# Performance work log

Measured on AMD Instinct MI355X. Metric: run time of the kernel, lower is better.

Reference implementation:

```python
import jax, jax.numpy as jnp
import numpy as np

N = 100000
E = 1600000
IN_C = 128
HID = 64
HEADS = 2
OUT_C = 64
Z = 16
NEG_SLOPE = 0.2


def _gat_layer(x, src, dst, W, a_src, a_dst, b, heads, d):
    # x: [N, in], W: [in, heads*d]
    h = (x @ W).reshape(-1, heads, d)                      # [N, H, d]
    alpha_s = (h * a_src).sum(-1)                          # [N, H]
    alpha_d = (h * a_dst).sum(-1)                          # [N, H]
    e = jax.nn.leaky_relu(alpha_s[src] + alpha_d[dst], NEG_SLOPE)  # [E, H]
    m = jax.ops.segment_max(e, dst, num_segments=N)        # [N, H]
    ex = jnp.exp(e - m[dst])
    denom = jax.ops.segment_sum(ex, dst, num_segments=N)   # [N, H]
    alpha = ex / (denom[dst] + 1e-16)                      # [E, H]
    out = jax.ops.segment_sum(h[src] * alpha[:, :, None], dst, num_segments=N)  # [N, H, d]
    return out.reshape(-1, heads * d) + b


def setup_inputs() -> dict:
    key = jax.random.key(0)
    ks = jax.random.split(key, 24)
    g = lambda k, shp, fan: jax.random.normal(k, shp, jnp.float32) * (1.0 / np.sqrt(fan))
    inp = {
        "x": jax.random.normal(ks[0], (N, IN_C), jnp.float32),
        "edge_index": jax.random.randint(ks[1], (2, E), 0, N, jnp.int64),
        "edge_attr": jax.random.normal(ks[2], (E, 8), jnp.float32),
        "eps": jax.random.normal(ks[3], (N, Z), jnp.float32),
        # GAT layer 1: heads=2, d=HID
        "W1": g(ks[4], (IN_C, HEADS * HID), IN_C),
        "a_src1": g(ks[5], (HEADS, HID), HID),
        "a_dst1": g(ks[6], (HEADS, HID), HID),
        "b1": jnp.zeros((HEADS * HID,), jnp.float32),
        # GAT layer 2: heads=1, d=OUT_C
        "W2": g(ks[7], (HEADS * HID, OUT_C), HEADS * HID),
        "a_src2": g(ks[8], (1, OUT_C), OUT_C),
        "a_dst2": g(ks[9], (1, OUT_C), OUT_C),
        "b2": jnp.zeros((OUT_C,), jnp.float32),
        # VAE
        "fc1_w": g(ks[10], (64, 128), 64), "fc1_b": jnp.zeros((128,), jnp.float32),
        "mu_w": g(ks[11], (128, Z), 128), "mu_b": jnp.zeros((Z,), jnp.float32),
        "lv_w": g(ks[12], (128, Z), 128), "lv_b": jnp.zeros((Z,), jnp.float32),
        "fc3_w": g(ks[13], (Z, 128), Z), "fc3_b": jnp.zeros((128,), jnp.float32),
        "fc4_w": g(ks[14], (128, 64), 128), "fc4_b": jnp.zeros((64,), jnp.float32),
    }
    return inp


def reference(x, edge_index, edge_attr, eps, W1, a_src1, a_dst1, b1, W2, a_src2, a_dst2, b2,
              fc1_w, fc1_b, mu_w, mu_b, lv_w, lv_b, fc3_w, fc3_b, fc4_w, fc4_b):
    src, dst = edge_index[0], edge_index[1]
    # GAT stack (edge_attr ignored: GATConv edge_dim=None)
    h = jax.nn.relu(_gat_layer(x, src, dst, W1, a_src1, a_dst1, b1, HEADS, HID))
    gat_out = _gat_layer(h, src, dst, W2, a_src2, a_dst2, b2, 1, OUT_C)  # [N, 64]
    # VAE
    h1 = jax.nn.relu(gat_out @ fc1_w + fc1_b)
    mu = h1 @ mu_w + mu_b
    logvar = h1 @ lv_w + lv_b
    lv = jnp.clip(logvar, -10.0, 10.0)
    z = mu + eps * jnp.exp(0.5 * lv)
    h3 = jax.nn.relu(z @ fc3_w + fc3_b)
    recon = h3 @ fc4_w + fc4_b
    return recon, mu, logvar, gat_out
```

## Files before the change

kernel.cpp:

```cpp
#include <hip/hip_runtime.h>
#include <hip/hip_bf16.h>

typedef __attribute__((ext_vector_type(8))) short bf16x8;
typedef __attribute__((ext_vector_type(4))) float f32x4;

__device__ __forceinline__ unsigned short f2b_bits(float x) {
    __hip_bfloat16 h = __float2bfloat16(x);
    unsigned short u;
    __builtin_memcpy(&u, &h, 2);
    return u;
}
__device__ __forceinline__ unsigned int pack2(float a, float b) {
    return (unsigned int)f2b_bits(a) | ((unsigned int)f2b_bits(b) << 16);
}
__device__ __forceinline__ float sx8(unsigned int w, int b) {
    return (float)((int)(w << (24 - 8 * b)) >> 24);
}

template<int FIN, int FOUT, int EPI, int HD, bool ABF, int ACT>
__global__ __launch_bounds__(256) void mfma_k(const void* __restrict__ Av,
                                              const float* __restrict__ W,
                                              const float* __restrict__ W2,
                                              const float* __restrict__ bias,
                                              const float* __restrict__ bias2,
                                              void* __restrict__ outv,
                                              void* __restrict__ out2,
                                              void* __restrict__ out3,
                                              float* __restrict__ scales,
                                              const float* __restrict__ asr,
                                              const float* __restrict__ adr,
                                              float* __restrict__ aso,
                                              float* __restrict__ ado,
                                              const float* __restrict__ epsp,
                                              int n)
{
    constexpr int KE = (FIN < 32) ? 32 : FIN;
    constexpr int KP = KE + 8;
    constexpr int KS = KE / 32;
    constexpr int NT = FOUT / 16;
    __shared__ __align__(16) unsigned short As[64 * KP];
    __shared__ __align__(16) unsigned short Wt[FOUT * KP];

    const int t  = threadIdx.x;
    const int m0 = blockIdx.x * 64;

    for (int idx = t; idx < 64 * (KE / 4); idx += 256) {
        int r  = idx / (KE / 4);
        int c4 = (idx % (KE / 4)) * 4;
        int row = m0 + r;
        unsigned int p0 = 0, p1 = 0;
        if (row < n && c4 < FIN) {
            if constexpr (ABF) {
                uint2 rv = *(const uint2*)((const unsigned short*)Av + (size_t)row * FIN + c4);
                p0 = rv.x; p1 = rv.y;
            } else {
                float4 v = *(const float4*)((const float*)Av + (size_t)row * FIN + c4);
                p0 = pack2(v.x, v.y); p1 = pack2(v.z, v.w);
            }
        }
        *(uint2*)(As + r * KP + c4) = make_uint2(p0, p1);
    }
    for (int idx = t; idx < KE * (FOUT / 4); idx += 256) {
        int k  = idx / (FOUT / 4);
        int c4 = (idx % (FOUT / 4)) * 4;
        float4 v = make_float4(0.f, 0.f, 0.f, 0.f);
        if (k < FIN) {
            if constexpr (EPI == 3) {
                v = (c4 < 16) ? *(const float4*)(W  + (size_t)k * 16 + c4)
                              : *(const float4*)(W2 + (size_t)k * 16 + (c4 - 16));
            } else {
                v = *(const float4*)(W + (size_t)k * FOUT + c4);
            }
        }
        Wt[(c4 + 0) * KP + k] = f2b_bits(v.x);
        Wt[(c4 + 1) * KP + k] = f2b_bits(v.y);
        Wt[(c4 + 2) * KP + k] = f2b_bits(v.z);
        Wt[(c4 + 3) * KP + k] = f2b_bits(v.w);
    }
    __syncthreads();

    const int w   = t >> 6;
    const int l   = t & 63;
    const int l15 = l & 15;
    const int g   = l >> 4;
    const int node = m0 + w * 16 + l15;

    f32x4 acc[NT];
    #pragma unroll
    for (int i = 0; i < NT; ++i) acc[i] = (f32x4){0.f, 0.f, 0.f, 0.f};

    #pragma unroll
    for (int ks = 0; ks < KS; ++ks) {
        bf16x8 nf = *(const bf16x8*)(As + (w * 16 + l15) * KP + ks * 32 + g * 8);
        #pragma unroll
        for (int tt = 0; tt < NT; ++tt) {
            bf16x8 wf = *(const bf16x8*)(Wt + (tt * 16 + l15) * KP + ks * 32 + g * 8);
            acc[tt] = __builtin_amdgcn_mfma_f32_16x16x32_bf16(wf, nf, acc[tt], 0, 0, 0);
        }
    }

    if constexpr (EPI == 0 || EPI == 1) {
        #pragma unroll
        for (int tt = 0; tt < NT; ++tt) {
            float4 bb = *(const float4*)(bias + 16 * tt + 4 * g);
            float o0 = acc[tt][0] + bb.x, o1 = acc[tt][1] + bb.y;
            float o2 = acc[tt][2] + bb.z, o3 = acc[tt][3] + bb.w;
            if (ACT == 1) {
                o0 = fmaxf(o0, 0.f); o1 = fmaxf(o1, 0.f);
                o2 = fmaxf(o2, 0.f); o3 = fmaxf(o3, 0.f);
            }
            if (node < n) {
                if constexpr (EPI == 0) {
                    *(float4*)((float*)outv + (size_t)node * FOUT + 16 * tt + 4 * g) =
                        make_float4(o0, o1, o2, o3);
                } else {
                    *(uint2*)((unsigned short*)outv + (size_t)node * FOUT + 16 * tt + 4 * g) =
                        make_uint2(pack2(o0, o1), pack2(o2, o3));
                }
            }
        }
    } else if constexpr (EPI == 2) {
        float amax = 0.f;
        float dsh[HD], ddh[HD];
        #pragma unroll
        for (int h = 0; h < HD; ++h) { dsh[h] = 0.f; ddh[h] = 0.f; }
        #pragma unroll
        for (int tt = 0; tt < NT; ++tt) {
            float4 av = *(const float4*)(asr + 16 * tt + 4 * g);
            float4 dv = *(const float4*)(adr + 16 * tt + 4 * g);
            const float* avp = (const float*)&av;
            const float* dvp = (const float*)&dv;
            const int h = (HD == 2) ? (tt / (NT / 2)) : 0;
            #pragma unroll
            for (int j = 0; j < 4; ++j) {
                float xv = acc[tt][j];
                amax = fmaxf(amax, fabsf(xv));
                dsh[h] = fmaf(xv, avp[j], dsh[h]);
                ddh[h] = fmaf(xv, dvp[j], ddh[h]);
            }
        }
        amax = fmaxf(amax, __shfl_xor(amax, 16, 64));
        amax = fmaxf(amax, __shfl_xor(amax, 32, 64));
        #pragma unroll
        for (int h = 0; h < HD; ++h) {
            dsh[h] += __shfl_xor(dsh[h], 16, 64);
            dsh[h] += __shfl_xor(dsh[h], 32, 64);
            ddh[h] += __shfl_xor(ddh[h], 16, 64);
            ddh[h] += __shfl_xor(ddh[h], 32, 64);
        }
        float invsc = amax > 0.f ? 127.f / amax : 0.f;
        if (node < n) {
            #pragma unroll
            for (int tt = 0; tt < NT; ++tt) {
                int q0 = __float2int_rn(acc[tt][0] * invsc);
                int q1 = __float2int_rn(acc[tt][1] * invsc);
                int q2 = __float2int_rn(acc[tt][2] * invsc);
                int q3 = __float2int_rn(acc[tt][3] * invsc);
                unsigned int pv = (q0 & 255) | ((q1 & 255) << 8) |
                                  ((q2 & 255) << 16) | ((q3 & 255) << 24);
                ((unsigned int*)outv)[(size_t)node * (FOUT / 4) + 4 * tt + g] = pv;
            }
            if (g == 0) {
                scales[node] = amax * (1.f / 127.f);
                #pragma unroll
                for (int h = 0; h < HD; ++h) {
                    aso[(size_t)node * HD + h] = dsh[h];
                    ado[(size_t)node * HD + h] = ddh[h];
                }
            }
        }
    } else {
        float4 mb = *(const float4*)(bias  + 4 * g);
        float4 lb = *(const float4*)(bias2 + 4 * g);
        float mu0 = acc[0][0] + mb.x, mu1 = acc[0][1] + mb.y;
        float mu2 = acc[0][2] + mb.z, mu3 = acc[0][3] + mb.w;
        float lv0 = acc[1][0] + lb.x, lv1 = acc[1][1] + lb.y;
        float lv2 = acc[1][2] + lb.z, lv3 = acc[1][3] + lb.w;
        if (node < n) {
            float4 ep = *(const float4*)(epsp + (size_t)node * 16 + 4 * g);
            float z0 = fmaf(ep.x, __expf(0.5f * fminf(fmaxf(lv0, -10.f), 10.f)), mu0);
            float z1 = fmaf(ep.y, __expf(0.5f * fminf(fmaxf(lv1, -10.f), 10.f)), mu1);
            float z2 = fmaf(ep.z, __expf(0.5f * fminf(fmaxf(lv2, -10.f), 10.f)), mu2);
            float z3 = fmaf(ep.w, __expf(0.5f * fminf(fmaxf(lv3, -10.f), 10.f)), mu3);
            *(float4*)((float*)outv + (size_t)node * 16 + 4 * g) = make_float4(mu0, mu1, mu2, mu3);
            *(float4*)((float*)out2 + (size_t)node * 16 + 4 * g) = make_float4(lv0, lv1, lv2, lv3);
            *(uint2*)((unsigned short*)out3 + (size_t)node * 16 + 4 * g) =
                make_uint2(pack2(z0, z1), pack2(z2, z3));
        }
    }
}

__global__ __launch_bounds__(256) void count_k(const int* __restrict__ ei, int* __restrict__ cnt,
                                               int E, int bshift)
{
    int e = blockIdx.x * 256 + threadIdx.x;
    if (e >= E) return;
    int s = ei[e], d = ei[E + e];
    atomicAdd(&cnt[d * 8 + (s >> bshift)], 1);
}

__global__ __launch_bounds__(256) void scanA_k(const int* __restrict__ cnt, int* __restrict__ incl,
                                               int* __restrict__ bsum, int m)
{
    __shared__ int sh[256];
    int i = blockIdx.x * 256 + threadIdx.x;
    int v = (i < m) ? cnt[i] : 0;
    sh[threadIdx.x] = v;
    __syncthreads();
    #pragma unroll
    for (int o = 1; o < 256; o <<= 1) {
        int t = (threadIdx.x >= o) ? sh[threadIdx.x - o] : 0;
        __syncthreads();
        sh[threadIdx.x] += t;
        __syncthreads();
    }
    if (i < m) incl[i] = sh[threadIdx.x];
    if (threadIdx.x == 255) bsum[blockIdx.x] = sh[255];
}

__global__ __launch_bounds__(512) void scanB_k(int* __restrict__ bsum, int nb)
{
    __shared__ int sh[512];
    __shared__ int carrysh;
    if (threadIdx.x == 0) carrysh = 0;
    __syncthreads();
    for (int base = 0; base < nb; base += 512) {
        int i = base + threadIdx.x;
        int v = (i < nb) ? bsum[i] : 0;
        sh[threadIdx.x] = v;
        __syncthreads();
        #pragma unroll
        for (int o = 1; o < 512; o <<= 1) {
            int t = (threadIdx.x >= o) ? sh[threadIdx.x - o] : 0;
            __syncthreads();
            sh[threadIdx.x] += t;
            __syncthreads();
        }
        int c = carrysh;
        if (i < nb) bsum[i] = c + sh[threadIdx.x] - v;
        __syncthreads();
        if (threadIdx.x == 511) carrysh = c + sh[511];
        __syncthreads();
    }
}

__global__ __launch_bounds__(256) void scanC_k(const int* __restrict__ cnt, const int* __restrict__ incl,
                                               const int* __restrict__ bsum, int* __restrict__ off,
                                               int* __restrict__ cursor, int m, int E)
{
    int i = blockIdx.x * 256 + threadIdx.x;
    if (i >= m) return;
    int v = incl[i] - cnt[i] + bsum[i >> 8];
    off[i] = v;
    cursor[i] = v;
    if (i == 0) off[m] = E;
}

__global__ __launch_bounds__(256) void scatter_k(const int* __restrict__ ei, int* __restrict__ cursor,
                                                 int* __restrict__ csr_src, int E, int n, int bshift)
{
    const int grp = blockIdx.x & 7;
    const int bin = blockIdx.x >> 3;
    const int bpg = gridDim.x >> 3;
    const int rsz = (n + 7) >> 3;
    const int lo = grp * rsz;
    const int hi = min(n, lo + rsz);
    const int stride = bpg * 256;
    for (int e = bin * 256 + threadIdx.x; e < E; e += stride) {
        int d = ei[E + e];
        if (d >= lo && d < hi) {
            int s = ei[e];
            int pos = atomicAdd(&cursor[d * 8 + (s >> bshift)], 1);
            csr_src[pos] = s;
        }
    }
}

template<int FEAT, int H, int ACT, bool OUTB>
__global__ __launch_bounds__(256) void gat_agg_k(const int* __restrict__ csr_src,
                                                 const int* __restrict__ off,
                                                 const float* __restrict__ as_,
                                                 const float* __restrict__ ad_,
                                                 const unsigned int* __restrict__ h8,
                                                 const float* __restrict__ sc,
                                                 const float* __restrict__ bias,
                                                 void* __restrict__ outv, int n)
{
    constexpr int LANES = 16;
    constexpr int FPL   = FEAT / LANES;
    constexpr int WPR   = FEAT / 4;
    constexpr int SUBL  = LANES / H;
    constexpr int NCH   = 4;
    const int tid = blockIdx.x * 256 + threadIdx.x;
    const int d = tid >> 4;
    if (d >= n) return;
    const int lane = threadIdx.x & 15;
    const int myhead = lane / SUBL;
    const int sl = lane % SUBL;
    const int start = off[d * 8], end = off[d * 8 + 8];
    const float adm = ad_[d * H + myhead];

    float vreg[NCH], sreg_sc[NCH]; int sreg[NCH];
    float m = -3.4e38f;
    #pragma unroll
    for (int c = 0; c < NCH; ++c) {
        int j = start + sl + c * SUBL;
        int s = 0; float v = -3.4e38f, scl = 0.f;
        if (j < end) {
            s = csr_src[j];
            v = as_[s * H + myhead] + adm;
            v = v > 0.f ? v : 0.2f * v;
            scl = sc[s];
        }
        sreg[c] = s; vreg[c] = v; sreg_sc[c] = scl;
        m = fmaxf(m, v);
    }
    for (int j = start + sl + NCH * SUBL; j < end; j += SUBL) {
        int s = csr_src[j];
        float v = as_[s * H + myhead] + adm;
        v = v > 0.f ? v : 0.2f * v;
        m = fmaxf(m, v);
    }
    #pragma unroll
    for (int o = SUBL / 2; o > 0; o >>= 1)
        m = fmaxf(m, __shfl_xor(m, o, SUBL));

    float ssum = 0.f;
    #pragma unroll
    for (int c = 0; c < NCH; ++c)
        if (start + sl + c * SUBL < end) ssum += __expf(vreg[c] - m);
    for (int j = start + sl + NCH * SUBL; j < end; j += SUBL) {
        int s = csr_src[j];
        float v = as_[s * H + myhead] + adm;
        v = v > 0.f ? v : 0.2f * v;
        ssum += __expf(v - m);
    }
    #pragma unroll
    for (int o = SUBL / 2; o > 0; o >>= 1)
        ssum += __shfl_xor(ssum, o, SUBL);
    const float inv = 1.f / (ssum + 1e-16f);

    float acc[FPL];
    #pragma unroll
    for (int k = 0; k < FPL; ++k) acc[k] = 0.f;

    auto body = [&](float a, int s) {
        if constexpr (FPL == 8) {
            uint2 r = ((const uint2*)(h8 + (size_t)s * WPR))[lane];
            acc[0] = fmaf(sx8(r.x, 0), a, acc[0]);
            acc[1] = fmaf(sx8(r.x, 1), a, acc[1]);
            acc[2] = fmaf(sx8(r.x, 2), a, acc[2]);
            acc[3] = fmaf(sx8(r.x, 3), a, acc[3]);
            acc[4] = fmaf(sx8(r.y, 0), a, acc[4]);
            acc[5] = fmaf(sx8(r.y, 1), a, acc[5]);
            acc[6] = fmaf(sx8(r.y, 2), a, acc[6]);
            acc[7] = fmaf(sx8(r.y, 3), a, acc[7]);
        } else {
            unsigned int r = (h8 + (size_t)s * WPR)[lane];
            acc[0] = fmaf(sx8(r, 0), a, acc[0]);
            acc[1] = fmaf(sx8(r, 1), a, acc[1]);
            acc[2] = fmaf(sx8(r, 2), a, acc[2]);
            acc[3] = fmaf(sx8(r, 3), a, acc[3]);
        }
    };

    const int nch = (end - start + SUBL - 1) / SUBL;
    for (int c = 0; c < nch; ++c) {
        const int j0 = start + c * SUBL;
        const int cnt = min(SUBL, end - j0);
        float myalpha = 0.f; int mysrc = 0;
        if (c < NCH) {
            mysrc = sreg[c];
            if (sl < cnt) myalpha = __expf(vreg[c] - m) * inv * sreg_sc[c];
        } else {
            if (sl < cnt) {
                mysrc = csr_src[j0 + sl];
                float v = as_[mysrc * H + myhead] + adm;
                v = v > 0.f ? v : 0.2f * v;
                myalpha = __expf(v - m) * inv * sc[mysrc];
            }
        }
        if (cnt == SUBL) {
            #pragma unroll
            for (int u = 0; u < SUBL; ++u) {
                float a = __shfl(myalpha, myhead * SUBL + u, LANES);
                int   s = __shfl(mysrc, u, LANES);
                body(a, s);
            }
        } else {
            for (int u = 0; u < cnt; ++u) {
                float a = __shfl(myalpha, myhead * SUBL + u, LANES);
                int   s = __shfl(mysrc, u, LANES);
                body(a, s);
            }
        }
    }

    if constexpr (OUTB) {
        float o[FPL];
        #pragma unroll
        for (int k = 0; k < FPL; ++k) {
            o[k] = acc[k] + bias[lane * FPL + k];
            if (ACT == 1) o[k] = fmaxf(o[k], 0.f);
        }
        uint4 pv;
        pv.x = pack2(o[0], o[1]); pv.y = pack2(o[2], o[3]);
        pv.z = pack2(o[4], o[5]); pv.w = pack2(o[6], o[7]);
        *(uint4*)((unsigned short*)outv + (size_t)d * FEAT + lane * FPL) = pv;
    } else {
        float* outf = (float*)outv;
        #pragma unroll
        for (int k = 0; k < FPL; ++k) {
            float o = acc[k] + bias[lane * FPL + k];
            if (ACT == 1) o = fmaxf(o, 0.f);
            outf[(size_t)d * FEAT + lane * FPL + k] = o;
        }
    }
}

extern "C" void kernel_launch(void* const* d_in, const int* in_sizes, int n_in,
                              void* d_out, int out_size, void* d_ws, size_t ws_size,
                              hipStream_t stream)
{
    const int n = in_sizes[0] / 128;
    const int E = in_sizes[1] / 2;
    const int m8 = n * 8;

    int bshift = 0;
    while (((n - 1) >> bshift) >= 8) ++bshift;

    const float* x   = (const float*)d_in[0];
    const int*   ei  = (const int*)d_in[1];
    const float* eps = (const float*)d_in[3];
    const float* W1  = (const float*)d_in[4];
    const float* as1w= (const float*)d_in[5];
    const float* ad1w= (const float*)d_in[6];
    const float* b1  = (const float*)d_in[7];
    const float* W2  = (const float*)d_in[8];
    const float* as2w= (const float*)d_in[9];
    const float* ad2w= (const float*)d_in[10];
    const float* b2  = (const float*)d_in[11];
    const float* fc1w= (const float*)d_in[12];
    const float* fc1b= (const float*)d_in[13];
    const float* muw = (const float*)d_in[14];
    const float* mub = (const float*)d_in[15];
    const float* lvw = (const float*)d_in[16];
    const float* lvb = (const float*)d_in[17];
    const float* fc3w= (const float*)d_in[18];
    const float* fc3b= (const float*)d_in[19];
    const float* fc4w= (const float*)d_in[20];
    const float* fc4b= (const float*)d_in[21];

    char* ws = (char*)d_ws;

    size_t oCnt   = 0;
    size_t oOff   = oCnt  + (size_t)m8 * 4;
    size_t oIncl  = oOff  + (size_t)(m8 + 1) * 4;
    size_t oCur   = oIncl + (size_t)m8 * 4;
    size_t oBsum  = oCur  + (size_t)m8 * 4;
    size_t oCsr   = oBsum + 4096 * 4;
    size_t oR1    = oCsr  + (size_t)E * 4;
    size_t oR2    = oR1   + (size_t)n * 256;
    size_t oR3    = oR2   + (size_t)n * 256;
    size_t oAS1   = oR3   + (size_t)n * 128;
    size_t oAD1   = oAS1  + (size_t)n * 2 * 4;
    size_t oAS2   = oAD1  + (size_t)n * 2 * 4;
    size_t oAD2   = oAS2  + (size_t)n * 4;
    size_t oSC1   = oAD2  + (size_t)n * 4;
    size_t oSC2   = oSC1  + (size_t)n * 4;
    (void)oSC2;

    int* cnt    = (int*)(ws + oCnt);
    int* off    = (int*)(ws + oOff);
    int* incl   = (int*)(ws + oIncl);
    int* cursor = (int*)(ws + oCur);
    int* bsum   = (int*)(ws + oBsum);
    int* csr    = (int*)(ws + oCsr);
    unsigned int*   h1q  = (unsigned int*)(ws + oR1);
    unsigned short* h1v  = (unsigned short*)(ws + oR1);
    unsigned short* hl2b = (unsigned short*)(ws + oR2);
    unsigned short* h3   = (unsigned short*)(ws + oR2);
    unsigned int*   h2q  = (unsigned int*)(ws + oR3);
    unsigned short* zb   = (unsigned short*)(ws + oR3);
    float* as1  = (float*)(ws + oAS1);
    float* ad1  = (float*)(ws + oAD1);
    float* as2  = (float*)(ws + oAS2);
    float* ad2  = (float*)(ws + oAD2);
    float* sc1  = (float*)(ws + oSC1);
    float* sc2  = (float*)(ws + oSC2);

    float* out     = (float*)d_out;
    float* o_recon = out;
    float* o_mu    = out + (size_t)n * 64;
    float* o_lv    = out + (size_t)n * 80;
    float* o_gat   = out + (size_t)n * 96;

    const int ebl  = (E + 255) / 256;
    const int nbS8 = (m8 + 255) / 256;
    const int abl  = (n * 16 + 255) / 256;
    const int g64  = (n + 63) / 64;

    hipMemsetAsync(cnt, 0, (size_t)m8 * 4, stream);
    count_k<<<ebl, 256, 0, stream>>>(ei, cnt, E, bshift);
    scanA_k<<<nbS8, 256, 0, stream>>>(cnt, incl, bsum, m8);
    scanB_k<<<1, 512, 0, stream>>>(bsum, nbS8);
    scanC_k<<<nbS8, 256, 0, stream>>>(cnt, incl, bsum, off, cursor, m8, E);
    scatter_k<<<1024, 256, 0, stream>>>(ei, cursor, csr, E, n, bshift);

    mfma_k<128, 128, 2, 2, false, 0><<<g64, 256, 0, stream>>>(
        x, W1, nullptr, nullptr, nullptr, h1q, nullptr, nullptr,
        sc1, as1w, ad1w, as1, ad1, nullptr, n);
    gat_agg_k<128, 2, 1, true><<<abl, 256, 0, stream>>>(
        csr, off, as1, ad1, h1q, sc1, b1, hl2b, n);

    mfma_k<128, 64, 2, 1, true, 0><<<g64, 256, 0, stream>>>(
        hl2b, W2, nullptr, nullptr, nullptr, h2q, nullptr, nullptr,
        sc2, as2w, ad2w, as2, ad2, nullptr, n);
    gat_agg_k<64, 1, 0, false><<<abl, 256, 0, stream>>>(
        csr, off, as2, ad2, h2q, sc2, b2, o_gat, n);

    mfma_k<64, 128, 1, 0, false, 1><<<g64, 256, 0, stream>>>(
        o_gat, fc1w, nullptr, fc1b, nullptr, h1v, nullptr, nullptr,
        nullptr, nullptr, nullptr, nullptr, nullptr, nullptr, n);
    mfma_k<128, 32, 3, 0, true, 0><<<g64, 256, 0, stream>>>(
        h1v, muw, lvw, mub, lvb, o_mu, o_lv, zb,
        nullptr, nullptr, nullptr, nullptr, nullptr, eps, n);
    mfma_k<16, 128, 1, 0, true, 1><<<g64, 256, 0, stream>>>(
        zb, fc3w, nullptr, fc3b, nullptr, h3, nullptr, nullptr,
        nullptr, nullptr, nullptr, nullptr, nullptr, nullptr, n);
    mfma_k<128, 64, 0, 0, true, 0><<<g64, 256, 0, stream>>>(
        h3, fc4w, nullptr, fc4b, nullptr, o_recon, nullptr, nullptr,
        nullptr, nullptr, nullptr, nullptr, nullptr, nullptr, n);
}
```

Before: 424.4 us.

## Partition edges by destination group before CSR scatter to avoid repeated edge scans

```diff
diff --git a/kernel.cpp b/kernel.cpp
--- a/kernel.cpp
+++ b/kernel.cpp
@@ -256,23 +256,57 @@
     if (i == 0) off[m] = E;
 }
 
-__global__ __launch_bounds__(256) void scatter_k(const int* __restrict__ ei, int* __restrict__ cursor,
-                                                 int* __restrict__ csr_src, int E, int n, int bshift)
-{
-    const int grp = blockIdx.x & 7;
+__global__ __launch_bounds__(256) void part_k(const int* __restrict__ ei, const int* __restrict__ off,
+                                              int* __restrict__ fill, int2* __restrict__ stage,
+                                              int E, int n, int bshift)
+{
+    __shared__ int lcnt[8];
+    __shared__ int lbase[8];
+    int g[4], s[4], d[4], rk[4];
+    const int e0 = blockIdx.x * 1024 + threadIdx.x;
+    if (threadIdx.x < 8) lcnt[threadIdx.x] = 0;
+    __syncthreads();
+    #pragma unroll
+    for (int k = 0; k < 4; ++k) {
+        int e = e0 + k * 256;
+        if (e < E) {
+            s[k] = ei[e]; d[k] = ei[E + e];
+            g[k] = d[k] >> bshift;
+            rk[k] = atomicAdd(&lcnt[g[k]], 1);
+        } else g[k] = -1;
+    }
+    __syncthreads();
+    if (threadIdx.x < 8) {
+        int c = lcnt[threadIdx.x];
+        lbase[threadIdx.x] = c ? atomicAdd(&fill[threadIdx.x], c) : 0;
+    }
+    __syncthreads();
+    #pragma unroll
+    for (int k = 0; k < 4; ++k) {
+        if (g[k] >= 0) {
+            int sb = off[(g[k] << bshift) * 8];
+            stage[sb + lbase[g[k]] + rk[k]] = make_int2(s[k], d[k]);
+        }
+    }
+}
+
+__global__ __launch_bounds__(256) void scatter2_k(const int2* __restrict__ stage,
+                                                  const int* __restrict__ off,
+                                                  int* __restrict__ cursor,
+                                                  int* __restrict__ csr, int n, int bshift)
+{
+    const int g = blockIdx.x & 7;
     const int bin = blockIdx.x >> 3;
     const int bpg = gridDim.x >> 3;
-    const int rsz = (n + 7) >> 3;
-    const int lo = grp * rsz;
-    const int hi = min(n, lo + rsz);
-    const int stride = bpg * 256;
-    for (int e = bin * 256 + threadIdx.x; e < E; e += stride) {
-        int d = ei[E + e];
-        if (d >= lo && d < hi) {
-            int s = ei[e];
-            int pos = atomicAdd(&cursor[d * 8 + (s >> bshift)], 1);
-            csr_src[pos] = s;
-        }
+    const int lo = g << bshift;
+    if (lo >= n) return;
+    const int hi = min(n, (g + 1) << bshift);
+    const int base = off[lo * 8];
+    const int count = off[hi * 8] - base;
+    for (int i = bin * 256 + threadIdx.x; i < count; i += bpg * 256) {
+        int2 e = stage[base + i];
+        int pos = atomicAdd(&cursor[e.y * 8 + (e.x >> bshift)], 1);
+        csr[pos] = e.x;
     }
 }
 
@@ -454,12 +488,14 @@
     char* ws = (char*)d_ws;
 
     size_t oCnt   = 0;
-    size_t oOff   = oCnt  + (size_t)m8 * 4;
+    size_t oFill  = oCnt  + (size_t)m8 * 4;
+    size_t oOff   = oFill + 8 * 4;
     size_t oIncl  = oOff  + (size_t)(m8 + 1) * 4;
     size_t oCur   = oIncl + (size_t)m8 * 4;
     size_t oBsum  = oCur  + (size_t)m8 * 4;
     size_t oCsr   = oBsum + 4096 * 4;
-    size_t oR1    = oCsr  + (size_t)E * 4;
+    size_t oStage = oCsr  + (size_t)E * 4;
+    size_t oR1    = oStage+ (size_t)E * 8;
     size_t oR2    = oR1   + (size_t)n * 256;
     size_t oR3    = oR2   + (size_t)n * 256;
     size_t oAS1   = oR3   + (size_t)n * 128;
@@ -468,14 +504,15 @@
     size_t oAD2   = oAS2  + (size_t)n * 4;
     size_t oSC1   = oAD2  + (size_t)n * 4;
     size_t oSC2   = oSC1  + (size_t)n * 4;
-    (void)oSC2;
 
     int* cnt    = (int*)(ws + oCnt);
+    int* fill   = (int*)(ws + oFill);
     int* off    = (int*)(ws + oOff);
     int* incl   = (int*)(ws + oIncl);
     int* cursor = (int*)(ws + oCur);
     int* bsum   = (int*)(ws + oBsum);
     int* csr    = (int*)(ws + oCsr);
+    int2* stage = (int2*)(ws + oStage);
     unsigned int*   h1q  = (unsigned int*)(ws + oR1);
     unsigned short* h1v  = (unsigned short*)(ws + oR1);
     unsigned short* hl2b = (unsigned short*)(ws + oR2);
@@ -499,13 +536,15 @@
     const int nbS8 = (m8 + 255) / 256;
     const int abl  = (n * 16 + 255) / 256;
     const int g64  = (n + 63) / 64;
-
-    hipMemsetAsync(cnt, 0, (size_t)m8 * 4, stream);
+    const int pblk = (E + 1023) / 1024;
+
+    hipMemsetAsync(cnt, 0, (size_t)m8 * 4 + 8 * 4, stream);
     count_k<<<ebl, 256, 0, stream>>>(ei, cnt, E, bshift);
     scanA_k<<<nbS8, 256, 0, stream>>>(cnt, incl, bsum, m8);
     scanB_k<<<1, 512, 0, stream>>>(bsum, nbS8);
     scanC_k<<<nbS8, 256, 0, stream>>>(cnt, incl, bsum, off, cursor, m8, E);
-    scatter_k<<<1024, 256, 0, stream>>>(ei, cursor, csr, E, n, bshift);
+    part_k<<<pblk, 256, 0, stream>>>(ei, off, fill, stage, E, n, bshift);
+    scatter2_k<<<1024, 256, 0, stream>>>(stage, off, cursor, csr, n, bshift);
 
     mfma_k<128, 128, 2, 2, false, 0><<<g64, 256, 0, stream>>>(
         x, W1, nullptr, nullptr, nullptr, h1q, nullptr, nullptr,
```

Result: slower. 452.9 us (+6.7%).
